# Kernel tuning notes

Measured on AMD Instinct MI355X. Metric: run time of the kernel, lower is better.

Reference implementation:

```python
import jax, jax.numpy as jnp
import numpy as np

NEG_SLOPE = 0.2


def setup_inputs() -> dict:
    key = jax.random.key(0)
    k1, k2, k3, k4, k5 = jax.random.split(key, 5)
    N, D, E = 10000, 128, 640000
    feat = jax.random.normal(k1, (N, D), dtype=jnp.float32)
    # nn.Linear weight [out_feats, in_feats]; scale like default init
    fc_weight = jax.random.normal(k2, (D, D), dtype=jnp.float32) / jnp.sqrt(jnp.float32(D))
    attn = jax.random.normal(k3, (1, 1, D), dtype=jnp.float32) * 0.1
    eps = jnp.zeros((1,), dtype=jnp.float32)
    src = jax.random.randint(k4, (E,), 0, N, dtype=jnp.int32)
    dst = jax.random.randint(k5, (E,), 0, N, dtype=jnp.int32)
    return {"feat": feat, "fc_weight": fc_weight, "attn": attn, "eps": eps,
            "src": src, "dst": dst}


def reference(feat, fc_weight, attn, eps, src, dst):
    N = feat.shape[0]
    # --- get_attention_tensor (attn_type='MX', num_heads=1) ---
    proj = feat @ fc_weight.T                      # [N, out]
    el = proj[src]                                  # [E, out] u side
    er = proj[dst]                                  # [E, out] v side
    a = attn.reshape(-1)                            # [out]
    e = jnp.sum(jax.nn.leaky_relu(el + er, NEG_SLOPE) * a, axis=-1)   # [E]
    gate = jax.nn.sigmoid(jnp.sum(el * er, axis=-1))                  # [E] sigmoid(u_dot_v)
    w = jax.nn.sigmoid(e * gate)                    # [E] final per-edge weight
    # --- message passing: u_mul_e('h','_edge_weight') with 'mean' reduce ---
    msg = feat[src] * w[:, None]                    # [E, D]
    neigh_sum = jax.ops.segment_sum(msg, dst, num_segments=N)         # [N, D]
    deg = jax.ops.segment_sum(jnp.ones_like(w), dst, num_segments=N)  # [N]
    neigh = neigh_sum / jnp.maximum(deg, 1.0)[:, None]                # mean; 0 for deg-0
    # --- node update ---
    rst = (1.0 + eps[0]) * feat + neigh
    return rst
```

## Files before the change

kernel.cpp:

```cpp
#include <hip/hip_runtime.h>

#define DD 128
#define CAP 128
#define BH 128

typedef unsigned short ushort_t;
typedef __attribute__((ext_vector_type(8))) short bf16x8;
typedef __attribute__((ext_vector_type(4))) float f32x4;

__device__ __forceinline__ unsigned short f2bf(float f) {
    unsigned u = __float_as_uint(f);
    u = (u + 0x7FFFu + ((u >> 16) & 1u)) >> 16;
    return (unsigned short)u;
}
__device__ __forceinline__ float bflo(unsigned v) { return __uint_as_float(v << 16); }
__device__ __forceinline__ float bfhi(unsigned v) { return __uint_as_float(v & 0xFFFF0000u); }
__device__ __forceinline__ unsigned pack2(float a, float b) {
    return (unsigned)f2bf(a) | ((unsigned)f2bf(b) << 16);
}
__device__ __forceinline__ bf16x8 cvt8(const float* __restrict__ p) {
    float4 f0 = *(const float4*)p;
    float4 f1 = *(const float4*)(p + 4);
    bf16x8 v;
    v[0] = (short)f2bf(f0.x); v[1] = (short)f2bf(f0.y);
    v[2] = (short)f2bf(f0.z); v[3] = (short)f2bf(f0.w);
    v[4] = (short)f2bf(f1.x); v[5] = (short)f2bf(f1.y);
    v[6] = (short)f2bf(f1.z); v[7] = (short)f2bf(f1.w);
    return v;
}

__global__ __launch_bounds__(256) void k1_hist_gemm_cast(
    const float* __restrict__ feat, const float* __restrict__ W,
    const float* __restrict__ attn, const int* __restrict__ dst,
    ushort_t* __restrict__ featb, ushort_t* __restrict__ projb,
    float* __restrict__ dotA, ushort_t* __restrict__ cnt,
    int N, int E, int GB, int CE)
{
    extern __shared__ unsigned h[];
    int b = (int)blockIdx.x;
    int NW = (N + 1) >> 1;
    if (b < BH) {
        for (int i = threadIdx.x; i < NW; i += 256) h[i] = 0;
        __syncthreads();
        int base = b * CE;
        for (int k = threadIdx.x; k < CE; k += 256) {
            int i = base + k;
            if (i < E) {
                int d = dst[i];
                atomicAdd(&h[d >> 1], (d & 1) ? 0x10000u : 1u);
            }
        }
        __syncthreads();
        ushort_t* crow = cnt + (size_t)b * N;
        for (int i = threadIdx.x; i < N; i += 256)
            crow[i] = (ushort_t)((h[i >> 1] >> ((i & 1) * 16)) & 0xFFFFu);
        return;
    }
    if (b < BH + GB) {
        int wave = (int)(((b - BH) * 256 + (int)threadIdx.x) >> 6);
        int lane = threadIdx.x & 63;
        int rowTile = wave >> 3;
        int colTile = wave & 7;
        if (rowTile * 16 >= N) return;
        int m = lane & 15;
        int quad = lane >> 4;
        const float* arow = feat + (size_t)(rowTile * 16 + m) * DD + quad * 8;
        const float* brow = W    + (size_t)(colTile * 16 + m) * DD + quad * 8;
        f32x4 acc = {0.f, 0.f, 0.f, 0.f};
#pragma unroll
        for (int ks = 0; ks < 4; ++ks) {
            bf16x8 a  = cvt8(arow + ks * 32);
            bf16x8 bb = cvt8(brow + ks * 32);
            acc = __builtin_amdgcn_mfma_f32_16x16x32_bf16(a, bb, acc, 0, 0, 0);
        }
        ushort_t* orow = projb + (size_t)(rowTile * 16 + quad * 4) * DD
                       + colTile * 16 + m;
#pragma unroll
        for (int r = 0; r < 4; ++r)
            orow[(size_t)r * DD] = f2bf(acc[r]);
        float av = 0.6f * attn[colTile * 16 + m];
        float d0 = av * acc[0], d1 = av * acc[1];
        float d2 = av * acc[2], d3 = av * acc[3];
#pragma unroll
        for (int o = 1; o < 16; o <<= 1) {
            d0 += __shfl_xor(d0, o); d1 += __shfl_xor(d1, o);
            d2 += __shfl_xor(d2, o); d3 += __shfl_xor(d3, o);
        }
        if (m == 0) {
            int rbase = rowTile * 16 + quad * 4;
            if (rbase + 3 < N) {
                atomicAdd(&dotA[rbase], d0);
                atomicAdd(&dotA[rbase + 1], d1);
                atomicAdd(&dotA[rbase + 2], d2);
                atomicAdd(&dotA[rbase + 3], d3);
            }
        }
        return;
    }
    size_t total = (size_t)N * DD;
    size_t idx = ((size_t)(b - BH - GB) * 256 + threadIdx.x) * 8;
    if (idx + 7 < total) {
        float4 f0 = *(const float4*)(feat + idx);
        float4 f1 = *(const float4*)(feat + idx + 4);
        uint4 o;
        o.x = pack2(f0.x, f0.y); o.y = pack2(f0.z, f0.w);
        o.z = pack2(f1.x, f1.y); o.w = pack2(f1.z, f1.w);
        *(uint4*)(featb + idx) = o;
    } else {
        for (size_t i = idx; i < total; ++i) featb[i] = f2bf(feat[i]);
    }
}

__global__ __launch_bounds__(256) void k2_scan(
    const ushort_t* __restrict__ cnt, ushort_t* __restrict__ offs,
    int* __restrict__ totals, int N)
{
    int bin = (int)blockIdx.x * 256 + (int)threadIdx.x;
    if (bin >= N) return;
    int run = 0;
#pragma unroll 8
    for (int blk = 0; blk < BH; ++blk) {
        int v = cnt[(size_t)blk * N + bin];
        offs[(size_t)blk * N + bin] = (ushort_t)run;
        run += v;
    }
    totals[bin] = run;
}

__global__ __launch_bounds__(256) void k3_scatter(
    const int* __restrict__ src, const int* __restrict__ dst,
    const ushort_t* __restrict__ offs, ushort_t* __restrict__ sorted,
    int N, int E, int CE)
{
    extern __shared__ unsigned h[];
    int b = (int)blockIdx.x;
    int NW = (N + 1) >> 1;
    for (int i = threadIdx.x; i < NW; i += 256) h[i] = 0;
    __syncthreads();
    const ushort_t* orow = offs + (size_t)b * N;
    int base = b * CE;
    for (int k = (int)threadIdx.x * 4; k < CE; k += 1024) {
        int i = base + k;
        if (i + 3 < E && k + 3 < CE) {
            int4 s4 = *(const int4*)(src + i);
            int4 d4 = *(const int4*)(dst + i);
            unsigned r0 = atomicAdd(&h[d4.x >> 1], (d4.x & 1) ? 0x10000u : 1u);
            unsigned r1 = atomicAdd(&h[d4.y >> 1], (d4.y & 1) ? 0x10000u : 1u);
            unsigned r2 = atomicAdd(&h[d4.z >> 1], (d4.z & 1) ? 0x10000u : 1u);
            unsigned r3 = atomicAdd(&h[d4.w >> 1], (d4.w & 1) ? 0x10000u : 1u);
            unsigned p0 = (unsigned)orow[d4.x] + ((r0 >> ((d4.x & 1) * 16)) & 0xFFFFu);
            unsigned p1 = (unsigned)orow[d4.y] + ((r1 >> ((d4.y & 1) * 16)) & 0xFFFFu);
            unsigned p2 = (unsigned)orow[d4.z] + ((r2 >> ((d4.z & 1) * 16)) & 0xFFFFu);
            unsigned p3 = (unsigned)orow[d4.w] + ((r3 >> ((d4.w & 1) * 16)) & 0xFFFFu);
            if (p0 < CAP) sorted[(size_t)d4.x * CAP + p0] = (ushort_t)s4.x;
            if (p1 < CAP) sorted[(size_t)d4.y * CAP + p1] = (ushort_t)s4.y;
            if (p2 < CAP) sorted[(size_t)d4.z * CAP + p2] = (ushort_t)s4.z;
            if (p3 < CAP) sorted[(size_t)d4.w * CAP + p3] = (ushort_t)s4.w;
        } else {
            for (int q = 0; q < 4 && k + q < CE; ++q) {
                int ii = base + k + q;
                if (ii < E) {
                    int d = dst[ii];
                    unsigned r = atomicAdd(&h[d >> 1], (d & 1) ? 0x10000u : 1u);
                    unsigned pos = (unsigned)orow[d]
                                 + ((r >> ((d & 1) * 16)) & 0xFFFFu);
                    if (pos < CAP) sorted[(size_t)d * CAP + pos] = (ushort_t)src[ii];
                }
            }
        }
    }
}

__global__ __launch_bounds__(256) void seg_agg(
    const ushort_t* __restrict__ projb, const ushort_t* __restrict__ featb,
    const float* __restrict__ feat, const float* __restrict__ attn,
    const float* __restrict__ dotA, const ushort_t* __restrict__ sorted,
    const int* __restrict__ totals, const float* __restrict__ eps,
    float* __restrict__ out, int N)
{
    int wid = (int)((blockIdx.x * (size_t)blockDim.x + threadIdx.x) >> 6);
    if (wid >= N) return;
    int lane = threadIdx.x & 63;
    int g   = lane >> 3;
    int sub = lane & 7;

    const uint4* projv = (const uint4*)projb;
    const uint4* featv = (const uint4*)featb;

    int m = min(totals[wid], CAP);
    const ushort_t* lst = sorted + (size_t)wid * CAP;

    uint4 ev0 = projv[(size_t)wid * 16 + 2 * sub];
    uint4 ev1 = projv[(size_t)wid * 16 + 2 * sub + 1];
    float er[16] = {
        bflo(ev0.x), bfhi(ev0.x), bflo(ev0.y), bfhi(ev0.y),
        bflo(ev0.z), bfhi(ev0.z), bflo(ev0.w), bfhi(ev0.w),
        bflo(ev1.x), bfhi(ev1.x), bflo(ev1.y), bfhi(ev1.y),
        bflo(ev1.z), bfhi(ev1.z), bflo(ev1.w), bfhi(ev1.w)};
    float av[16];
#pragma unroll
    for (int k = 0; k < 16; ++k) av[k] = 0.4f * attn[16 * sub + k];
    float dAr = dotA[wid];
    float c[16];
#pragma unroll
    for (int k = 0; k < 16; ++k) c[k] = 0.f;

    uint4 apv0, apv1, afv0, afv1; float adAl = 0.f;
    uint4 bpv0, bpv1, bfv0, bfv1; float bdAl = 0.f;

    auto ldst = [&](int idx, uint4& pv0, uint4& pv1, uint4& fv0, uint4& fv1,
                    float& dAl) {
        int s = (idx < m) ? (int)lst[idx] : 0;
        pv0 = projv[(size_t)s * 16 + 2 * sub];
        pv1 = projv[(size_t)s * 16 + 2 * sub + 1];
        fv0 = featv[(size_t)s * 16 + 2 * sub];
        fv1 = featv[(size_t)s * 16 + 2 * sub + 1];
        dAl = dotA[s];
    };

    int i = g;
    if (i < m)     ldst(i,     apv0, apv1, afv0, afv1, adAl);
    if (i + 8 < m) ldst(i + 8, bpv0, bpv1, bfv0, bfv1, bdAl);

    while (i < m) {
        uint4 cpv0, cpv1, cfv0, cfv1; float cdAl;
        ldst(i + 16, cpv0, cpv1, cfv0, cfv1, cdAl);
        float el[16] = {
            bflo(apv0.x), bfhi(apv0.x), bflo(apv0.y), bfhi(apv0.y),
            bflo(apv0.z), bfhi(apv0.z), bflo(apv0.w), bfhi(apv0.w),
            bflo(apv1.x), bfhi(apv1.x), bflo(apv1.y), bfhi(apv1.y),
            bflo(apv1.z), bfhi(apv1.z), bflo(apv1.w), bfhi(apv1.w)};
        float gp = 0.f, ad = 0.f;
#pragma unroll
        for (int k = 0; k < 16; ++k) {
            gp = fmaf(el[k], er[k], gp);
            ad = fmaf(fabsf(el[k] + er[k]), av[k], ad);
        }
#pragma unroll
        for (int o = 1; o <= 4; o <<= 1) {
            gp += __shfl_xor(gp, o);
            ad += __shfl_xor(ad, o);
        }
        float ep = adAl + dAr + ad;
        float gate = 1.f / (1.f + __expf(-gp));
        float w = 1.f / (1.f + __expf(-ep * gate));
        float fl[16] = {
            bflo(afv0.x), bfhi(afv0.x), bflo(afv0.y), bfhi(afv0.y),
            bflo(afv0.z), bfhi(afv0.z), bflo(afv0.w), bfhi(afv0.w),
            bflo(afv1.x), bfhi(afv1.x), bflo(afv1.y), bfhi(afv1.y),
            bflo(afv1.z), bfhi(afv1.z), bflo(afv1.w), bfhi(afv1.w)};
#pragma unroll
        for (int k = 0; k < 16; ++k) c[k] = fmaf(fl[k], w, c[k]);
        apv0 = bpv0; apv1 = bpv1; afv0 = bfv0; afv1 = bfv1; adAl = bdAl;
        bpv0 = cpv0; bpv1 = cpv1; bfv0 = cfv0; bfv1 = cfv1; bdAl = cdAl;
        i += 8;
    }
#pragma unroll
    for (int o = 8; o <= 32; o <<= 1) {
#pragma unroll
        for (int k = 0; k < 16; ++k) c[k] += __shfl_xor(c[k], o);
    }
    if (g == 0) {
        float inv = 1.f / fmaxf((float)m, 1.f);
        float sc = 1.f + eps[0];
        const f32x4* fsrc = (const f32x4*)feat + (size_t)wid * 32 + 4 * sub;
        f32x4* od = (f32x4*)out + (size_t)wid * 32 + 4 * sub;
#pragma unroll
        for (int q = 0; q < 4; ++q) {
            f32x4 f = __builtin_nontemporal_load(&fsrc[q]);
            f32x4 o;
            o[0] = fmaf(sc, f[0], c[4 * q] * inv);
            o[1] = fmaf(sc, f[1], c[4 * q + 1] * inv);
            o[2] = fmaf(sc, f[2], c[4 * q + 2] * inv);
            o[3] = fmaf(sc, f[3], c[4 * q + 3] * inv);
            __builtin_nontemporal_store(o, &od[q]);
        }
    }
}

extern "C" void kernel_launch(void* const* d_in, const int* in_sizes, int n_in,
                              void* d_out, int out_size, void* d_ws, size_t ws_size,
                              hipStream_t stream) {
    const float* feat = (const float*)d_in[0];
    const float* W    = (const float*)d_in[1];
    const float* attn = (const float*)d_in[2];
    const float* eps  = (const float*)d_in[3];
    const int*   src  = (const int*)d_in[4];
    const int*   dst  = (const int*)d_in[5];
    int N = in_sizes[0] / DD;
    int E = in_sizes[4];

    ushort_t* projb  = (ushort_t*)d_ws;
    ushort_t* featb  = projb + (size_t)N * DD;
    ushort_t* sorted = featb + (size_t)N * DD;
    ushort_t* cnt    = sorted + (size_t)N * CAP;
    ushort_t* offs   = cnt + (size_t)BH * N;
    int*      totals = (int*)(offs + (size_t)BH * N);
    float*    dotA   = (float*)(totals + N);

    int CE = (E + BH - 1) / BH;
    int GB = (((N + 15) / 16) * 8 + 3) / 4;
    int CB = (N * DD + 2047) / 2048;
    size_t ldsB = (size_t)((N + 1) / 2) * sizeof(unsigned);

    k1_hist_gemm_cast<<<BH + GB + CB, 256, ldsB, stream>>>(
        feat, W, attn, dst, featb, projb, dotA, cnt, N, E, GB, CE);
    k2_scan<<<(N + 255) / 256, 256, 0, stream>>>(cnt, offs, totals, N);
    k3_scatter<<<BH, 256, ldsB, stream>>>(src, dst, offs, sorted, N, E, CE);
    seg_agg<<<(N * 64 + 255) / 256, 256, 0, stream>>>(
        projb, featb, feat, attn, dotA, sorted, totals, eps,
        (float*)d_out, N);
}
```

Baseline: 139.4 us.

## Reuse A fragments across column tiles and move feature cast into scan kernel

The GEMM now gives each wave one 16-row tile and loops over all 8 column tiles. The A fragment is loaded and converted once and reused, and the attention dot product is accumulated in registers, so the float atomics on dotA become plain stores. The bf16 cast of feat moves from the first kernel into the scan kernel, which runs as extra blocks beside the scan. This aims to cut redundant feat loads, atomic traffic and load imbalance in the first kernel. In exchange there are fewer GEMM waves with more serial work each, and the scan kernel grows larger. Plain stores to dotA assume dotA is no longer zero-initialized for accumulation, which is consistent with each wave now owning whole rows.

```diff
diff --git a/kernel.cpp b/kernel.cpp
--- a/kernel.cpp
+++ b/kernel.cpp
@@ -29,17 +29,16 @@
     return v;
 }
 
-__global__ __launch_bounds__(256) void k1_hist_gemm_cast(
+__global__ __launch_bounds__(256) void k1_hist_gemm(
     const float* __restrict__ feat, const float* __restrict__ W,
     const float* __restrict__ attn, const int* __restrict__ dst,
-    ushort_t* __restrict__ featb, ushort_t* __restrict__ projb,
-    float* __restrict__ dotA, ushort_t* __restrict__ cnt,
-    int N, int E, int GB, int CE)
+    ushort_t* __restrict__ projb, float* __restrict__ dotA,
+    ushort_t* __restrict__ cnt, int N, int E, int CE)
 {
     extern __shared__ unsigned h[];
     int b = (int)blockIdx.x;
-    int NW = (N + 1) >> 1;
     if (b < BH) {
+        int NW = (N + 1) >> 1;
         for (int i = threadIdx.x; i < NW; i += 256) h[i] = 0;
         __syncthreads();
         int base = b * CE;
@@ -56,49 +55,73 @@
             crow[i] = (ushort_t)((h[i >> 1] >> ((i & 1) * 16)) & 0xFFFFu);
         return;
     }
-    if (b < BH + GB) {
-        int wave = (int)(((b - BH) * 256 + (int)threadIdx.x) >> 6);
-        int lane = threadIdx.x & 63;
-        int rowTile = wave >> 3;
-        int colTile = wave & 7;
-        if (rowTile * 16 >= N) return;
-        int m = lane & 15;
-        int quad = lane >> 4;
-        const float* arow = feat + (size_t)(rowTile * 16 + m) * DD + quad * 8;
-        const float* brow = W    + (size_t)(colTile * 16 + m) * DD + quad * 8;
+    int rowTile = (b - BH) * 4 + ((int)threadIdx.x >> 6);
+    if (rowTile * 16 >= N) return;
+    int lane = threadIdx.x & 63;
+    int m = lane & 15;
+    int quad = lane >> 4;
+    const float* arow = feat + (size_t)(rowTile * 16 + m) * DD + quad * 8;
+    bf16x8 afr[4];
+#pragma unroll
+    for (int ks = 0; ks < 4; ++ks) afr[ks] = cvt8(arow + ks * 32);
+    float dacc0 = 0.f, dacc1 = 0.f, dacc2 = 0.f, dacc3 = 0.f;
+#pragma unroll
+    for (int ct = 0; ct < 8; ++ct) {
+        const float* brow = W + (size_t)(ct * 16 + m) * DD + quad * 8;
         f32x4 acc = {0.f, 0.f, 0.f, 0.f};
 #pragma unroll
         for (int ks = 0; ks < 4; ++ks) {
-            bf16x8 a  = cvt8(arow + ks * 32);
             bf16x8 bb = cvt8(brow + ks * 32);
-            acc = __builtin_amdgcn_mfma_f32_16x16x32_bf16(a, bb, acc, 0, 0, 0);
+            acc = __builtin_amdgcn_mfma_f32_16x16x32_bf16(afr[ks], bb, acc, 0, 0, 0);
         }
         ushort_t* orow = projb + (size_t)(rowTile * 16 + quad * 4) * DD
-                       + colTile * 16 + m;
+                       + ct * 16 + m;
 #pragma unroll
         for (int r = 0; r < 4; ++r)
             orow[(size_t)r * DD] = f2bf(acc[r]);
-        float av = 0.6f * attn[colTile * 16 + m];
-        float d0 = av * acc[0], d1 = av * acc[1];
-        float d2 = av * acc[2], d3 = av * acc[3];
-#pragma unroll
-        for (int o = 1; o < 16; o <<= 1) {
-            d0 += __shfl_xor(d0, o); d1 += __shfl_xor(d1, o);
-            d2 += __shfl_xor(d2, o); d3 += __shfl_xor(d3, o);
-        }
-        if (m == 0) {
-            int rbase = rowTile * 16 + quad * 4;
-            if (rbase + 3 < N) {
-                atomicAdd(&dotA[rbase], d0);
-                atomicAdd(&dotA[rbase + 1], d1);
-                atomicAdd(&dotA[rbase + 2], d2);
-                atomicAdd(&dotA[rbase + 3], d3);
-            }
-        }
+        float av = 0.6f * attn[ct * 16 + m];
+        dacc0 = fmaf(av, acc[0], dacc0);
+        dacc1 = fmaf(av, acc[1], dacc1);
+        dacc2 = fmaf(av, acc[2], dacc2);
+        dacc3 = fmaf(av, acc[3], dacc3);
+    }
+#pragma unroll
+    for (int o = 1; o < 16; o <<= 1) {
+        dacc0 += __shfl_xor(dacc0, o); dacc1 += __shfl_xor(dacc1, o);
+        dacc2 += __shfl_xor(dacc2, o); dacc3 += __shfl_xor(dacc3, o);
+    }
+    if (m == 0) {
+        int rbase = rowTile * 16 + quad * 4;
+        if (rbase + 3 < N) {
+            dotA[rbase]     = dacc0;
+            dotA[rbase + 1] = dacc1;
+            dotA[rbase + 2] = dacc2;
+            dotA[rbase + 3] = dacc3;
+        }
+    }
+}
+
+__global__ __launch_bounds__(256) void k2_scan_cast(
+    const float* __restrict__ feat, const ushort_t* __restrict__ cnt,
+    ushort_t* __restrict__ offs, int* __restrict__ totals,
+    ushort_t* __restrict__ featb, int N, int SC)
+{
+    int b = (int)blockIdx.x;
+    if (b < SC) {
+        int bin = b * 256 + (int)threadIdx.x;
+        if (bin >= N) return;
+        int run = 0;
+#pragma unroll 8
+        for (int blk = 0; blk < BH; ++blk) {
+            int v = cnt[(size_t)blk * N + bin];
+            offs[(size_t)blk * N + bin] = (ushort_t)run;
+            run += v;
+        }
+        totals[bin] = run;
         return;
     }
     size_t total = (size_t)N * DD;
-    size_t idx = ((size_t)(b - BH - GB) * 256 + threadIdx.x) * 8;
+    size_t idx = ((size_t)(b - SC) * 256 + threadIdx.x) * 8;
     if (idx + 7 < total) {
         float4 f0 = *(const float4*)(feat + idx);
         float4 f1 = *(const float4*)(feat + idx + 4);
@@ -109,22 +132,6 @@
     } else {
         for (size_t i = idx; i < total; ++i) featb[i] = f2bf(feat[i]);
     }
-}
-
-__global__ __launch_bounds__(256) void k2_scan(
-    const ushort_t* __restrict__ cnt, ushort_t* __restrict__ offs,
-    int* __restrict__ totals, int N)
-{
-    int bin = (int)blockIdx.x * 256 + (int)threadIdx.x;
-    if (bin >= N) return;
-    int run = 0;
-#pragma unroll 8
-    for (int blk = 0; blk < BH; ++blk) {
-        int v = cnt[(size_t)blk * N + bin];
-        offs[(size_t)blk * N + bin] = (ushort_t)run;
-        run += v;
-    }
-    totals[bin] = run;
 }
 
 __global__ __launch_bounds__(256) void k3_scatter(
@@ -299,13 +306,15 @@
     float*    dotA   = (float*)(totals + N);
 
     int CE = (E + BH - 1) / BH;
-    int GB = (((N + 15) / 16) * 8 + 3) / 4;
+    int GB = ((N + 15) / 16 + 3) / 4;
+    int SC = (N + 255) / 256;
     int CB = (N * DD + 2047) / 2048;
     size_t ldsB = (size_t)((N + 1) / 2) * sizeof(unsigned);
 
-    k1_hist_gemm_cast<<<BH + GB + CB, 256, ldsB, stream>>>(
-        feat, W, attn, dst, featb, projb, dotA, cnt, N, E, GB, CE);
-    k2_scan<<<(N + 255) / 256, 256, 0, stream>>>(cnt, offs, totals, N);
+    k1_hist_gemm<<<BH + GB, 256, ldsB, stream>>>(
+        feat, W, attn, dst, projb, dotA, cnt, N, E, CE);
+    k2_scan_cast<<<SC + CB, 256, 0, stream>>>(
+        feat, cnt, offs, totals, featb, N, SC);
     k3_scatter<<<BH, 256, ldsB, stream>>>(src, dst, offs, sorted, N, E, CE);
     seg_agg<<<(N * 64 + 255) / 256, 256, 0, stream>>>(
         projb, featb, feat, attn, dotA, sorted, totals, eps,
```

After: 138.1 us. About the same (-1.0%).
